# Kernel tuning notes

Hardware: AMD Instinct MI355X
Metric: run time of the kernel (lower is better)

Reference implementation:

```python
import jax, jax.numpy as jnp
import numpy as np

N, E, G = 20000, 100000, 32
HID, HEADS, HC = 64, 8, 64  # hidden, heads, per-head channels (PyG: out_channels per head)
L, K = 3, 4


def setup_inputs() -> dict:
    key = jax.random.key(0)
    ks = jax.random.split(key, 20)
    rn = lambda k, s, sc=0.05: jax.random.normal(k, s, jnp.float32) * sc
    HO = HEADS * HC  # 512
    return {
        "x": jax.random.uniform(ks[0], (N, 7), jnp.float32),
        "edge_attr": jax.random.normal(ks[1], (E, 4), jnp.float32),
        "means": jax.random.normal(ks[2], (K, 8), jnp.float32),
        "log_stds": jnp.zeros((K, 8), jnp.float32),
        "sp_W": rn(ks[3], (K, HID), 0.3), "sp_b": jnp.zeros((HID,), jnp.float32),
        "ne_W": rn(ks[4], (7, HID), 0.3), "ne_b": jnp.zeros((HID,), jnp.float32),
        "ee_W": rn(ks[5], (4, HID), 0.3), "ee_b": jnp.zeros((HID,), jnp.float32),
        "Wq": rn(ks[6], (L, HID, HO)), "bq": jnp.zeros((L, HO), jnp.float32),
        "Wk": rn(ks[7], (L, HID, HO)), "bk": jnp.zeros((L, HO), jnp.float32),
        "Wv": rn(ks[8], (L, HID, HO)), "bv": jnp.zeros((L, HO), jnp.float32),
        "We": rn(ks[9], (L, HID, HO)), "be": jnp.zeros((L, HO), jnp.float32),
        "Ws": rn(ks[10], (L, HID, HID)), "bs": jnp.zeros((L, HID), jnp.float32),
        "eu_W": rn(ks[11], (L, 3 * HID, HID)), "eu_b": jnp.zeros((L, HID), jnp.float32),
        "rW1": rn(ks[12], (2 * HID, HID)), "rb1": jnp.zeros((HID,), jnp.float32),
        "rW2": rn(ks[13], (HID, HID)), "rb2": jnp.zeros((HID,), jnp.float32),
        "rW3": rn(ks[14], (HID, 2)), "rb3": jnp.zeros((2,), jnp.float32),
        "edge_index": jax.random.randint(ks[15], (2, E), 0, N, jnp.int32),
        "batch": jnp.sort(jax.random.randint(ks[16], (N,), 0, G, jnp.int32)),
        "num_graphs": G,
    }


def reference(x, edge_attr, means, log_stds, sp_W, sp_b, ne_W, ne_b, ee_W, ee_b,
              Wq, bq, Wk, bk, Wv, bv, We, be, Ws, bs, eu_W, eu_b,
              rW1, rb1, rW2, rb2, rW3, rb3, edge_index, batch, num_graphs):
    n = x.shape[0]
    src, dst = edge_index[0], edge_index[1]

    # ---- SpatialGaussianEncoder (dropout is identity in eval) ----
    p = x[:, :4]
    sl, sr = p[src, :2], p[src, 2:4]
    dl, dr = p[dst, :2], p[dst, 2:4]
    rel = jnp.stack([dl - sl, dl - sr, dr - sl, dr - sr], axis=1)  # [E,4,2]
    dist = jnp.linalg.norm(rel, axis=-1)                           # [E,4]
    ang = jnp.arctan2(rel[..., 1], rel[..., 0])                    # [E,4]
    u = jnp.stack([dist, ang], axis=-1).reshape(-1, 8)             # [E,8] (d,a)x4
    std = jnp.exp(log_stds) + 1e-6                                 # [K,8]
    z = (u[:, None, :] - means[None]) / std[None]                  # [E,K,8]
    w = jnp.exp(-0.5 * jnp.sum(z * z, axis=-1))                    # [E,K]
    sp = jax.nn.relu(w @ sp_W + sp_b)                              # [E,HID]

    h = jax.nn.relu(x @ ne_W + ne_b)                               # [N,HID]
    ea = jax.nn.relu(edge_attr @ ee_W + ee_b) + sp                 # [E,HID]

    scale = 1.0 / float(np.sqrt(HC))
    for l in range(L):
        # PyG TransformerConv(hidden, hidden, heads=8, edge_dim=hidden, concat=False)
        q = (h @ Wq[l] + bq[l]).reshape(n, HEADS, HC)
        k = (h @ Wk[l] + bk[l]).reshape(n, HEADS, HC)
        v = (h @ Wv[l] + bv[l]).reshape(n, HEADS, HC)
        e = (ea @ We[l] + be[l]).reshape(-1, HEADS, HC)
        kj = k[src] + e                                            # [E,H,C]
        alpha = jnp.einsum('ehc,ehc->eh', q[dst], kj) * scale      # [E,H]
        m = jax.ops.segment_max(alpha, dst, num_segments=n)
        ex = jnp.exp(alpha - m[dst])
        den = jax.ops.segment_sum(ex, dst, num_segments=n)
        a = ex / (den[dst] + 1e-16)                                # scatter-softmax over dst
        msg = a[:, :, None] * (v[src] + e)                         # [E,H,C]
        out = jax.ops.segment_sum(msg, dst, num_segments=n).mean(axis=1)  # concat=False -> head mean
        h = jax.nn.relu(out + h @ Ws[l] + bs[l])                   # skip (root_weight) + F.relu
        ef = jnp.concatenate([h[src], h[dst], ea], axis=1)         # [E,3*HID]
        ea = jax.nn.relu(ef @ eu_W[l] + eu_b[l])

    # ---- per-graph masked-mean pooling == segment mean ----
    cn = jnp.maximum(jax.ops.segment_sum(jnp.ones((n,), x.dtype), batch, num_segments=num_graphs), 1.0)
    node_pool = jax.ops.segment_sum(h, batch, num_segments=num_graphs) / cn[:, None]
    eb = batch[src]
    ce = jnp.maximum(jax.ops.segment_sum(jnp.ones((src.shape[0],), x.dtype), eb, num_segments=num_graphs), 1.0)
    edge_pool = jax.ops.segment_sum(ea, eb, num_segments=num_graphs) / ce[:, None]
    g = jnp.concatenate([node_pool, edge_pool], axis=1)            # [G,2*HID]

    h1 = jax.nn.relu(g @ rW1 + rb1)
    h2 = jax.nn.relu(h1 @ rW2 + rb2)
    return jnp.tanh(h2 @ rW3 + rb3)                                # [G,2]
```

## Files before the change

### kernel.cpp

```cpp
#include <hip/hip_runtime.h>
#include <hip/hip_bf16.h>
#include <cstdint>
#include <cstddef>



__global__ void __launch_bounds__(256) k_node_embed(
    const float* __restrict__ x, const float* __restrict__ neW, const float* __restrict__ neb,
    float* __restrict__ h, int N)
{
    int idx = blockIdx.x * 256 + threadIdx.x;
    int n = idx >> 6, c = idx & 63;
    if (n >= N) return;
    float acc = neb[c];
    #pragma unroll
    for (int j = 0; j < 7; ++j) acc += x[(size_t)n * 7 + j] * neW[j * 64 + c];
    h[(size_t)n * 64 + c] = fmaxf(acc, 0.f);
}

__global__ void __launch_bounds__(256) k_edge_w(
    const float* __restrict__ x,
    const float* __restrict__ means, const float* __restrict__ log_stds,
    const int* __restrict__ src, const int* __restrict__ dst,
    float* __restrict__ wbuf, int E)
{
    int e = blockIdx.x * 256 + threadIdx.x;
    if (e >= E) return;
    int s = src[e], d = dst[e];
    const float* ps = x + (size_t)s * 7;
    const float* pd = x + (size_t)d * 7;
    float slx = ps[0], sly = ps[1], srx = ps[2], sry = ps[3];
    float dlx = pd[0], dly = pd[1], drx = pd[2], dry = pd[3];
    float u[8];
    float rx, ry;
    rx = dlx - slx; ry = dly - sly; u[0] = sqrtf(rx*rx + ry*ry); u[1] = atan2f(ry, rx);
    rx = dlx - srx; ry = dly - sry; u[2] = sqrtf(rx*rx + ry*ry); u[3] = atan2f(ry, rx);
    rx = drx - slx; ry = dry - sly; u[4] = sqrtf(rx*rx + ry*ry); u[5] = atan2f(ry, rx);
    rx = drx - srx; ry = dry - sry; u[6] = sqrtf(rx*rx + ry*ry); u[7] = atan2f(ry, rx);
    #pragma unroll
    for (int kk = 0; kk < 4; ++kk) {
        float ssum = 0.f;
        #pragma unroll
        for (int dd = 0; dd < 8; ++dd) {
            float stdv = expf(log_stds[kk*8+dd]) + 1e-6f;
            float z = (u[dd] - means[kk*8+dd]) / stdv;
            ssum += z * z;
        }
        wbuf[(size_t)e*4 + kk] = expf(-0.5f * ssum);
    }
}

__global__ void __launch_bounds__(256) k_edge_ea(
    const float* __restrict__ edge_attr, const float* __restrict__ wbuf,
    const float* __restrict__ spW, const float* __restrict__ spb,
    const float* __restrict__ eeW, const float* __restrict__ eeb,
    float* __restrict__ ea, int E)
{
    int idx = blockIdx.x * 256 + threadIdx.x;
    int e = idx >> 6, c = idx & 63;
    if (e >= E) return;
    float acce = eeb[c];
    #pragma unroll
    for (int j = 0; j < 4; ++j) acce += edge_attr[(size_t)e*4 + j] * eeW[j*64 + c];
    float accs = spb[c];
    #pragma unroll
    for (int j = 0; j < 4; ++j) accs += wbuf[(size_t)e*4 + j] * spW[j*64 + c];
    ea[(size_t)e*64 + c] = fmaxf(acce, 0.f) + fmaxf(accs, 0.f);
}


__global__ void __launch_bounds__(256) k_hist(
    const int* __restrict__ dst, int* __restrict__ deg, int E)
{
    int e = blockIdx.x * 256 + threadIdx.x;
    if (e < E) atomicAdd(deg + dst[e], 1);
}

__global__ void __launch_bounds__(1024) k_scan(
    const int* __restrict__ deg, int* __restrict__ ptr, int* __restrict__ headw, int N)
{
    __shared__ int part[1024];
    int t = threadIdx.x;
    int per = (N + 1023) / 1024;
    int s = 0;
    for (int i = 0; i < per; ++i) { int idx = t*per + i; if (idx < N) s += deg[idx]; }
    part[t] = s;
    __syncthreads();
    for (int off = 1; off < 1024; off <<= 1) {
        int v = (t >= off) ? part[t - off] : 0;
        __syncthreads();
        part[t] += v;
        __syncthreads();
    }
    int base = (t > 0) ? part[t - 1] : 0;
    for (int i = 0; i < per; ++i) {
        int idx = t*per + i;
        if (idx < N) { ptr[idx] = base; headw[idx] = base; base += deg[idx]; }
    }
    if (t == 1023) ptr[N] = part[1023];
}

__global__ void __launch_bounds__(256) k_scatter(
    const int* __restrict__ dst, const int* __restrict__ src, const int* __restrict__ batch,
    int* __restrict__ headw, int* __restrict__ perm, int* __restrict__ srcg,
    int* __restrict__ ieb, int E)
{
    int e = blockIdx.x * 256 + threadIdx.x;
    if (e < E) {
        int s = src[e];
        int pos = atomicAdd(headw + dst[e], 1);
        perm[pos] = e;
        srcg[pos] = s;
        ieb[e] = batch[s];
    }
}


__global__ void __launch_bounds__(256) k_wprod_all(
    const float* __restrict__ Wq, const float* __restrict__ bq,
    const float* __restrict__ Wk, const float* __restrict__ We,
    float* __restrict__ Mk, float* __restrict__ Me,
    float* __restrict__ bqk, float* __restrict__ bqe)
{
    int h = blockIdx.x;
    int which = blockIdx.y;
    int l = blockIdx.z;
    const float* Wq_l = Wq + (size_t)l * 64 * 512;
    const float* bq_l = bq + (size_t)l * 512;
    const float* Wx_l = (which ? We : Wk) + (size_t)l * 64 * 512;
    float* M  = (which ? Me : Mk) + (size_t)l * 64 * 512;
    float* bM = (which ? bqe : bqk) + (size_t)l * 512;
    __shared__ float wq_s[65][64];
    __shared__ float wx_s[64][65];
    int tid = threadIdx.x;
    for (int i = tid; i < 4096; i += 256) {
        int r = i >> 6, c2 = i & 63;
        wq_s[r][c2] = Wq_l[(size_t)r*512 + h*64 + c2];
        wx_s[r][c2] = Wx_l[(size_t)r*512 + h*64 + c2];
    }
    if (tid < 64) wq_s[64][tid] = bq_l[h*64 + tid];
    __syncthreads();
    int j = tid & 63, cg = tid >> 6;
    for (int c = cg*16; c < cg*16 + 16; ++c) {
        float s = 0.f;
        #pragma unroll 8
        for (int c2 = 0; c2 < 64; ++c2) s += wq_s[c][c2] * wx_s[j][c2];
        M[(size_t)c*512 + h*64 + j] = s;
    }
    if (tid < 64) {
        float s = 0.f;
        #pragma unroll 8
        for (int c2 = 0; c2 < 64; ++c2) s += wq_s[64][c2] * wx_s[tid][c2];
        bM[h*64 + tid] = s;
    }
}

__global__ void __launch_bounds__(64) k_wqb_all(
    const float* __restrict__ Wq, const float* __restrict__ bq,
    const float* __restrict__ bk, const float* __restrict__ be,
    float* __restrict__ wqb, float* __restrict__ cb)
{
    int l = blockIdx.x;
    const float* Wq_l = Wq + (size_t)l * 64 * 512;
    const float* bq_l = bq + (size_t)l * 512;
    const float* bk_l = bk + (size_t)l * 512;
    const float* be_l = be + (size_t)l * 512;
    float* wqb_l = wqb + (size_t)l * 512;
    float* cb_l  = cb + (size_t)l * 8;
    int c = threadIdx.x;
    for (int h = 0; h < 8; ++h) {
        float s = 0.f;
        for (int c2 = 0; c2 < 64; ++c2)
            s += Wq_l[(size_t)c*512 + h*64 + c2] * (bk_l[h*64+c2] + be_l[h*64+c2]);
        wqb_l[c*8 + h] = s;
    }
    if (c < 8) {
        float s = 0.f;
        for (int c2 = 0; c2 < 64; ++c2)
            s += bq_l[c*64 + c2] * (bk_l[c*64+c2] + be_l[c*64+c2]);
        cb_l[c] = s;
    }
}

__global__ void __launch_bounds__(256) k_qb(
    const float* __restrict__ h, const float* __restrict__ wqb, const float* __restrict__ cb,
    float* __restrict__ qbv, int N)
{
    int idx = blockIdx.x * 256 + threadIdx.x;
    int n = idx >> 3, hh = idx & 7;
    if (n >= N) return;
    float s = cb[hh];
    #pragma unroll 8
    for (int c = 0; c < 64; ++c) s += h[(size_t)n*64 + c] * wqb[c*8 + hh];
    qbv[(size_t)n*8 + hh] = s;
}


__global__ void __launch_bounds__(256) k_gemm512_r32(
    const float* __restrict__ X, const float* __restrict__ W, const float* __restrict__ bias,
    float* __restrict__ Y, int M)
{
    __shared__ __align__(16) float xs[32][64];
    int tid = threadIdx.x;
    int r0 = blockIdx.x * 32;
    for (int i = tid; i < 2048; i += 256) {
        int r = i >> 6, c = i & 63;
        int rr = r0 + r;
        xs[r][c] = (rr < M) ? X[(size_t)rr * 64 + c] : 0.f;
    }
    __syncthreads();
    int wv = tid >> 6, lane = tid & 63;
    int c0 = lane * 8;
    float acc[8][8];
    float4 b0 = *(const float4*)(bias + c0);
    float4 b1 = *(const float4*)(bias + c0 + 4);
    #pragma unroll
    for (int t = 0; t < 8; ++t) {
        acc[t][0]=b0.x; acc[t][1]=b0.y; acc[t][2]=b0.z; acc[t][3]=b0.w;
        acc[t][4]=b1.x; acc[t][5]=b1.y; acc[t][6]=b1.z; acc[t][7]=b1.w;
    }
    #pragma unroll 2
    for (int j = 0; j < 64; ++j) {
        float4 wa = *(const float4*)(W + (size_t)j*512 + c0);
        float4 wb = *(const float4*)(W + (size_t)j*512 + c0 + 4);
        #pragma unroll
        for (int t = 0; t < 8; ++t) {
            float a = xs[wv*8 + t][j];
            acc[t][0] += a*wa.x; acc[t][1] += a*wa.y; acc[t][2] += a*wa.z; acc[t][3] += a*wa.w;
            acc[t][4] += a*wb.x; acc[t][5] += a*wb.y; acc[t][6] += a*wb.z; acc[t][7] += a*wb.w;
        }
    }
    #pragma unroll
    for (int t = 0; t < 8; ++t) {
        int r = r0 + wv*8 + t;
        if (r < M) {
            float4 o0 = {acc[t][0],acc[t][1],acc[t][2],acc[t][3]};
            float4 o1 = {acc[t][4],acc[t][5],acc[t][6],acc[t][7]};
            *(float4*)(Y + (size_t)r*512 + c0)     = o0;
            *(float4*)(Y + (size_t)r*512 + c0 + 4) = o1;
        }
    }
}


__global__ void __launch_bounds__(256) k_attn_alpha2(
    const float* __restrict__ qk, const float* __restrict__ qe2, const float* __restrict__ qbv,
    const float* __restrict__ ea, const float* __restrict__ hbuf,
    const int* __restrict__ ptr, const int* __restrict__ perm, const int* __restrict__ srcg,
    float* __restrict__ alpha, float* __restrict__ mbuf, float* __restrict__ dbuf, int N)
{
    int wv = threadIdx.x >> 6, lane = threadIdx.x & 63;
    int n = blockIdx.x * 4 + wv;
    if (n >= N) return;
    int h = lane >> 3, p = lane & 7;
    int b = ptr[n], e_ = ptr[n + 1];
    const float4* xp = (const float4*)(qk + (size_t)n*512 + lane*8);
    float4 x0 = xp[0], x1 = xp[1];
    const float4* gp = (const float4*)(qe2 + (size_t)n*512 + lane*8);
    float4 g0 = gp[0], g1 = gp[1];
    float qbh = qbv[(size_t)n*8 + h];
    float m = -3.4e38f, den = 0.f;
    for (int it = b; it < e_; ++it) {
        int s = srcg[it];
        int e = perm[it];
        const float4* hp = (const float4*)(hbuf + (size_t)s*64 + p*8);
        float4 h0 = hp[0], h1 = hp[1];
        const float4* ap = (const float4*)(ea + (size_t)e*64 + p*8);
        float4 a0 = ap[0], a1 = ap[1];
        float t = x0.x*h0.x + x0.y*h0.y + x0.z*h0.z + x0.w*h0.w
                + x1.x*h1.x + x1.y*h1.y + x1.z*h1.z + x1.w*h1.w
                + g0.x*a0.x + g0.y*a0.y + g0.z*a0.z + g0.w*a0.w
                + g1.x*a1.x + g1.y*a1.y + g1.z*a1.z + g1.w*a1.w;
        t += __shfl_xor(t, 1);
        t += __shfl_xor(t, 2);
        t += __shfl_xor(t, 4);
        float al = 0.125f * (t + qbh);
        float mn = fmaxf(m, al);
        den = den * expf(m - mn) + expf(al - mn);
        m = mn;
        if (p == 0) alpha[(size_t)it*8 + h] = al;
    }
    if (p == 0) {
        mbuf[(size_t)n*8 + h] = m;
        dbuf[(size_t)n*8 + h] = den;
    }
}

__global__ void __launch_bounds__(256) k_attn_agg2(
    const float* __restrict__ alpha, const float* __restrict__ mbuf, const float* __restrict__ dbuf,
    const float* __restrict__ ea, const float* __restrict__ hbuf,
    const int* __restrict__ ptr, const int* __restrict__ perm, const int* __restrict__ srcg,
    float* __restrict__ hagg, float* __restrict__ tbuf, float* __restrict__ sbuf, int N)
{
    int wv = threadIdx.x >> 6, lane = threadIdx.x & 63;
    int n = blockIdx.x * 4 + wv;
    if (n >= N) return;
    int h = lane >> 3, p = lane & 7;
    int b = ptr[n], e_ = ptr[n + 1];
    float m = mbuf[(size_t)n*8 + h];
    float inv = 0.125f / (dbuf[(size_t)n*8 + h] + 1e-16f);
    float hacc[8], tacc[8];
    #pragma unroll
    for (int i = 0; i < 8; ++i) { hacc[i] = 0.f; tacc[i] = 0.f; }
    float sacc = 0.f;
    for (int it = b; it < e_; ++it) {
        int s = srcg[it];
        int e = perm[it];
        float a = expf(alpha[(size_t)it*8 + h] - m) * inv;
        sacc += a;
        const float4* hp = (const float4*)(hbuf + (size_t)s*64 + p*8);
        float4 h0 = hp[0], h1 = hp[1];
        const float4* ap = (const float4*)(ea + (size_t)e*64 + p*8);
        float4 a0 = ap[0], a1 = ap[1];
        hacc[0] += a*h0.x; hacc[1] += a*h0.y; hacc[2] += a*h0.z; hacc[3] += a*h0.w;
        hacc[4] += a*h1.x; hacc[5] += a*h1.y; hacc[6] += a*h1.z; hacc[7] += a*h1.w;
        tacc[0] += a*a0.x; tacc[1] += a*a0.y; tacc[2] += a*a0.z; tacc[3] += a*a0.w;
        tacc[4] += a*a1.x; tacc[5] += a*a1.y; tacc[6] += a*a1.z; tacc[7] += a*a1.w;
    }
    float4 o;
    o = {hacc[0],hacc[1],hacc[2],hacc[3]}; *(float4*)(hagg + (size_t)n*512 + lane*8)     = o;
    o = {hacc[4],hacc[5],hacc[6],hacc[7]}; *(float4*)(hagg + (size_t)n*512 + lane*8 + 4) = o;
    o = {tacc[0],tacc[1],tacc[2],tacc[3]}; *(float4*)(tbuf + (size_t)n*512 + lane*8)     = o;
    o = {tacc[4],tacc[5],tacc[6],tacc[7]}; *(float4*)(tbuf + (size_t)n*512 + lane*8 + 4) = o;
    if (p == 0) sbuf[(size_t)n*8 + h] = sacc;
}

__global__ void __launch_bounds__(256) k_nf_gemm2(
    const float* __restrict__ tbuf, const float* __restrict__ hagg,
    const float* __restrict__ We, const float* __restrict__ Wv,
    float* __restrict__ pbuf, int N)
{
    __shared__ float As[64][132];
    __shared__ __align__(16) float Wt[64][64];
    int tid = threadIdx.x;
    int y = blockIdx.y;
    int n0 = blockIdx.x * 128;
    int wv = tid >> 6, lane = tid & 63;
    int rg = lane >> 3, cg = lane & 7;
    int c0 = cg * 8;
    int rbase = wv * 32 + rg * 4;
    float acc[4][8];
    #pragma unroll
    for (int t = 0; t < 4; ++t)
        #pragma unroll
        for (int i = 0; i < 8; ++i) acc[t][i] = 0.f;
    #pragma unroll
    for (int round = 0; round < 2; ++round) {
        const float* A = round ? hagg : tbuf;
        const float* W = round ? Wv : We;
        {
            int rt = tid & 127;
            int n = n0 + rt;
            int jh = (tid >> 7) * 32;
            if (n < N) {
                const float* ap = A + (size_t)n*512 + y*64;
                #pragma unroll
                for (int j4 = 0; j4 < 8; ++j4) {
                    int j = jh + j4 * 4;
                    float4 a = *(const float4*)(ap + j);
                    As[j+0][rt] = a.x; As[j+1][rt] = a.y;
                    As[j+2][rt] = a.z; As[j+3][rt] = a.w;
                }
            } else {
                #pragma unroll
                for (int j4 = 0; j4 < 8; ++j4) {
                    int j = jh + j4 * 4;
                    As[j+0][rt] = 0.f; As[j+1][rt] = 0.f;
                    As[j+2][rt] = 0.f; As[j+3][rt] = 0.f;
                }
            }
            #pragma unroll
            for (int i = 0; i < 4; ++i) {
                int idx = tid + i * 256;
                int j = idx >> 4, c4 = (idx & 15) * 4;
                *(float4*)&Wt[j][c4] = *(const float4*)(W + (size_t)j*512 + y*64 + c4);
            }
        }
        __syncthreads();
        #pragma unroll 4
        for (int j = 0; j < 64; ++j) {
            float4 av = *(const float4*)&As[j][rbase];
            float4 w0 = *(const float4*)&Wt[j][c0];
            float4 w1 = *(const float4*)&Wt[j][c0 + 4];
            acc[0][0] += av.x*w0.x; acc[0][1] += av.x*w0.y; acc[0][2] += av.x*w0.z; acc[0][3] += av.x*w0.w;
            acc[0][4] += av.x*w1.x; acc[0][5] += av.x*w1.y; acc[0][6] += av.x*w1.z; acc[0][7] += av.x*w1.w;
            acc[1][0] += av.y*w0.x; acc[1][1] += av.y*w0.y; acc[1][2] += av.y*w0.z; acc[1][3] += av.y*w0.w;
            acc[1][4] += av.y*w1.x; acc[1][5] += av.y*w1.y; acc[1][6] += av.y*w1.z; acc[1][7] += av.y*w1.w;
            acc[2][0] += av.z*w0.x; acc[2][1] += av.z*w0.y; acc[2][2] += av.z*w0.z; acc[2][3] += av.z*w0.w;
            acc[2][4] += av.z*w1.x; acc[2][5] += av.z*w1.y; acc[2][6] += av.z*w1.z; acc[2][7] += av.z*w1.w;
            acc[3][0] += av.w*w0.x; acc[3][1] += av.w*w0.y; acc[3][2] += av.w*w0.z; acc[3][3] += av.w*w0.w;
            acc[3][4] += av.w*w1.x; acc[3][5] += av.w*w1.y; acc[3][6] += av.w*w1.z; acc[3][7] += av.w*w1.w;
        }
        __syncthreads();
    }
    float* out = pbuf + (size_t)y * N * 64;
    #pragma unroll
    for (int t = 0; t < 4; ++t) {
        int n = n0 + rbase + t;
        if (n < N) {
            float4 o0 = {acc[t][0],acc[t][1],acc[t][2],acc[t][3]};
            float4 o1 = {acc[t][4],acc[t][5],acc[t][6],acc[t][7]};
            *(float4*)(out + (size_t)n*64 + c0)     = o0;
            *(float4*)(out + (size_t)n*64 + c0 + 4) = o1;
        }
    }
}

__global__ void __launch_bounds__(256) k_nf_reduce2(
    const float* __restrict__ pbuf, const float* __restrict__ hin,
    const float* __restrict__ sbuf, const float* __restrict__ Ws,
    const float* __restrict__ be, const float* __restrict__ bv,
    const float* __restrict__ bs, float* __restrict__ hnext, int N)
{
    int idx = blockIdx.x * 256 + threadIdx.x;
    int n = idx >> 6, cc = idx & 63;
    if (n >= N) return;
    float a = bs[cc];
    #pragma unroll
    for (int y = 0; y < 8; ++y) a += pbuf[(size_t)y*N*64 + (size_t)n*64 + cc];
    float hv = hin[(size_t)n*64 + cc];
    #pragma unroll 8
    for (int j = 0; j < 64; ++j) a += __shfl(hv, j) * Ws[(size_t)j*64 + cc];
    #pragma unroll
    for (int h = 0; h < 8; ++h)
        a += sbuf[(size_t)n*8 + h] * (be[h*64 + cc] + bv[h*64 + cc]);
    hnext[(size_t)n*64 + cc] = fmaxf(a, 0.f);
}

__global__ void __launch_bounds__(256) k_eu_pre(
    const float* __restrict__ h, const float* __restrict__ euW,
    float* __restrict__ hw, int N)
{
    __shared__ float As[64][132];
    __shared__ __align__(16) float Wt[64][64];
    int tid = threadIdx.x;
    int y = blockIdx.y;
    int n0 = blockIdx.x * 128;
    {
        int rt = tid & 127;
        int n = n0 + rt;
        int jh = (tid >> 7) * 32;
        if (n < N) {
            const float* ap = h + (size_t)n*64;
            #pragma unroll
            for (int j4 = 0; j4 < 8; ++j4) {
                int j = jh + j4 * 4;
                float4 a = *(const float4*)(ap + j);
                As[j+0][rt] = a.x; As[j+1][rt] = a.y;
                As[j+2][rt] = a.z; As[j+3][rt] = a.w;
            }
        } else {
            #pragma unroll
            for (int j4 = 0; j4 < 8; ++j4) {
                int j = jh + j4 * 4;
                As[j+0][rt] = 0.f; As[j+1][rt] = 0.f;
                As[j+2][rt] = 0.f; As[j+3][rt] = 0.f;
            }
        }
        #pragma unroll
        for (int i = 0; i < 4; ++i) {
            int idx = tid + i * 256;
            *(float4*)&Wt[idx >> 4][(idx & 15) * 4] =
                *(const float4*)(euW + (size_t)y*4096 + idx * 4);
        }
    }
    __syncthreads();
    int wv = tid >> 6, lane = tid & 63;
    int rg = lane >> 3, cg = lane & 7;
    int c0 = cg * 8;
    int rbase = wv * 32 + rg * 4;
    float acc[4][8];
    #pragma unroll
    for (int t = 0; t < 4; ++t)
        #pragma unroll
        for (int i = 0; i < 8; ++i) acc[t][i] = 0.f;
    #pragma unroll 4
    for (int j = 0; j < 64; ++j) {
        float4 av = *(const float4*)&As[j][rbase];
        float4 w0 = *(const float4*)&Wt[j][c0];
        float4 w1 = *(const float4*)&Wt[j][c0 + 4];
        acc[0][0] += av.x*w0.x; acc[0][1] += av.x*w0.y; acc[0][2] += av.x*w0.z; acc[0][3] += av.x*w0.w;
        acc[0][4] += av.x*w1.x; acc[0][5] += av.x*w1.y; acc[0][6] += av.x*w1.z; acc[0][7] += av.x*w1.w;
        acc[1][0] += av.y*w0.x; acc[1][1] += av.y*w0.y; acc[1][2] += av.y*w0.z; acc[1][3] += av.y*w0.w;
        acc[1][4] += av.y*w1.x; acc[1][5] += av.y*w1.y; acc[1][6] += av.y*w1.z; acc[1][7] += av.y*w1.w;
        acc[2][0] += av.z*w0.x; acc[2][1] += av.z*w0.y; acc[2][2] += av.z*w0.z; acc[2][3] += av.z*w0.w;
        acc[2][4] += av.z*w1.x; acc[2][5] += av.z*w1.y; acc[2][6] += av.z*w1.z; acc[2][7] += av.z*w1.w;
        acc[3][0] += av.w*w0.x; acc[3][1] += av.w*w0.y; acc[3][2] += av.w*w0.z; acc[3][3] += av.w*w0.w;
        acc[3][4] += av.w*w1.x; acc[3][5] += av.w*w1.y; acc[3][6] += av.w*w1.z; acc[3][7] += av.w*w1.w;
    }
    #pragma unroll
    for (int t = 0; t < 4; ++t) {
        int n = n0 + rbase + t;
        if (n < N) {
            float4 o0 = {acc[t][0],acc[t][1],acc[t][2],acc[t][3]};
            float4 o1 = {acc[t][4],acc[t][5],acc[t][6],acc[t][7]};
            *(float4*)(hw + (size_t)n*128 + y*64 + c0)     = o0;
            *(float4*)(hw + (size_t)n*128 + y*64 + c0 + 4) = o1;
        }
    }
}

__global__ void __launch_bounds__(256) k_edge_update2(
    const float* __restrict__ hw, const float* __restrict__ ea,
    const float* __restrict__ euW2, const float* __restrict__ eub,
    const int* __restrict__ src, const int* __restrict__ dst,
    float* __restrict__ ea2, int E)
{
    __shared__ float As[64][132];
    __shared__ __align__(16) float Wt[64][64];
    __shared__ int sid[128], did[128];
    int tid = threadIdx.x;
    int e0 = blockIdx.x * 128;
    if (tid < 128) {
        int e = e0 + tid; if (e >= E) e = E - 1;
        sid[tid] = src[e]; did[tid] = dst[e];
    }
    {
        int et = tid & 127;
        int e = e0 + et; if (e >= E) e = E - 1;
        const float* ap = ea + (size_t)e * 64;
        int jh = (tid >> 7) * 32;
        #pragma unroll
        for (int j4 = 0; j4 < 8; ++j4) {
            int j = jh + j4 * 4;
            float4 a = *(const float4*)(ap + j);
            As[j+0][et] = a.x; As[j+1][et] = a.y;
            As[j+2][et] = a.z; As[j+3][et] = a.w;
        }
        #pragma unroll
        for (int i = 0; i < 4; ++i) {
            int idx = tid + i * 256;
            *(float4*)&Wt[idx >> 4][(idx & 15) * 4] = *(const float4*)(euW2 + idx * 4);
        }
    }
    __syncthreads();
    int wv = tid >> 6, lane = tid & 63;
    int rg = lane >> 3, cg = lane & 7;
    int c0 = cg * 8;
    int rbase = wv * 32 + rg * 4;
    float acc[4][8];
    float4 b0 = *(const float4*)(eub + c0);
    float4 b1 = *(const float4*)(eub + c0 + 4);
    #pragma unroll
    for (int t = 0; t < 4; ++t) {
        acc[t][0]=b0.x; acc[t][1]=b0.y; acc[t][2]=b0.z; acc[t][3]=b0.w;
        acc[t][4]=b1.x; acc[t][5]=b1.y; acc[t][6]=b1.z; acc[t][7]=b1.w;
    }
    #pragma unroll 4
    for (int j = 0; j < 64; ++j) {
        float4 av = *(const float4*)&As[j][rbase];
        float4 w0 = *(const float4*)&Wt[j][c0];
        float4 w1 = *(const float4*)&Wt[j][c0 + 4];
        acc[0][0] += av.x*w0.x; acc[0][1] += av.x*w0.y; acc[0][2] += av.x*w0.z; acc[0][3] += av.x*w0.w;
        acc[0][4] += av.x*w1.x; acc[0][5] += av.x*w1.y; acc[0][6] += av.x*w1.z; acc[0][7] += av.x*w1.w;
        acc[1][0] += av.y*w0.x; acc[1][1] += av.y*w0.y; acc[1][2] += av.y*w0.z; acc[1][3] += av.y*w0.w;
        acc[1][4] += av.y*w1.x; acc[1][5] += av.y*w1.y; acc[1][6] += av.y*w1.z; acc[1][7] += av.y*w1.w;
        acc[2][0] += av.z*w0.x; acc[2][1] += av.z*w0.y; acc[2][2] += av.z*w0.z; acc[2][3] += av.z*w0.w;
        acc[2][4] += av.z*w1.x; acc[2][5] += av.z*w1.y; acc[2][6] += av.z*w1.z; acc[2][7] += av.z*w1.w;
        acc[3][0] += av.w*w0.x; acc[3][1] += av.w*w0.y; acc[3][2] += av.w*w0.z; acc[3][3] += av.w*w0.w;
        acc[3][4] += av.w*w1.x; acc[3][5] += av.w*w1.y; acc[3][6] += av.w*w1.z; acc[3][7] += av.w*w1.w;
    }
    #pragma unroll
    for (int t = 0; t < 4; ++t) {
        int e = e0 + rbase + t;
        if (e < E) {
            int s = sid[rbase + t], d = did[rbase + t];
            const float4* sp = (const float4*)(hw + (size_t)s*128 + c0);
            const float4* dp = (const float4*)(hw + (size_t)d*128 + 64 + c0);
            float4 s0 = sp[0], s1 = sp[1];
            float4 d0 = dp[0], d1 = dp[1];
            float4 o0 = {fmaxf(acc[t][0]+s0.x+d0.x,0.f), fmaxf(acc[t][1]+s0.y+d0.y,0.f),
                         fmaxf(acc[t][2]+s0.z+d0.z,0.f), fmaxf(acc[t][3]+s0.w+d0.w,0.f)};
            float4 o1 = {fmaxf(acc[t][4]+s1.x+d1.x,0.f), fmaxf(acc[t][5]+s1.y+d1.y,0.f),
                         fmaxf(acc[t][6]+s1.z+d1.z,0.f), fmaxf(acc[t][7]+s1.w+d1.w,0.f)};
            *(float4*)(ea2 + (size_t)e*64 + c0)     = o0;
            *(float4*)(ea2 + (size_t)e*64 + c0 + 4) = o1;
        }
    }
}


__global__ void __launch_bounds__(64) k_node_pool(
    const float* __restrict__ h, const int* __restrict__ batch,
    float* __restrict__ npool, float* __restrict__ cn, int N)
{
    int lane = threadIdx.x;
    int n0 = blockIdx.x * 64;
    float acc = 0.f; int cur = -1; int run = 0;
    for (int i = 0; i < 64; ++i) {
        int n = n0 + i;
        if (n >= N) break;
        int b = batch[n];
        if (b != cur) {
            if (cur >= 0) {
                atomicAdd(npool + (size_t)cur*64 + lane, acc);
                if (lane == 0) atomicAdd(cn + cur, (float)run);
            }
            cur = b; acc = 0.f; run = 0;
        }
        acc += h[(size_t)n*64 + lane];
        ++run;
    }
    if (cur >= 0) {
        atomicAdd(npool + (size_t)cur*64 + lane, acc);
        if (lane == 0) atomicAdd(cn + cur, (float)run);
    }
}

__global__ void __launch_bounds__(256) k_edge_pool2(
    const float* __restrict__ ea, const int* __restrict__ ieb,
    float* __restrict__ rep, int E)
{
    __shared__ float pool_s[32][64];
    __shared__ float cnt_s[32];
    int tid = threadIdx.x;
    for (int i = tid; i < 2048; i += 256) ((float*)pool_s)[i] = 0.f;
    if (tid < 32) cnt_s[tid] = 0.f;
    __syncthreads();
    int wv = tid >> 6, lane = tid & 63;
    int base = blockIdx.x * 64 + wv * 16;
    int b16[16]; float v16[16];
    #pragma unroll
    for (int u = 0; u < 16; ++u) {
        int e = base + u;
        bool ok = (e < E);
        b16[u] = ok ? ieb[e] : -1;
        v16[u] = ok ? ea[(size_t)e*64 + lane] : 0.f;
    }
    #pragma unroll
    for (int u = 0; u < 16; ++u) {
        if (b16[u] >= 0) {
            atomicAdd(&pool_s[b16[u]][lane], v16[u]);
            if (lane == 0) atomicAdd(&cnt_s[b16[u]], 1.f);
        }
    }
    __syncthreads();
    float* myrep = rep + (size_t)(blockIdx.x & 7) * 2080;
    for (int i = tid; i < 2048; i += 256) atomicAdd(myrep + i, ((float*)pool_s)[i]);
    if (tid < 32) atomicAdd(myrep + 2048 + tid, cnt_s[tid]);
}

__global__ void __launch_bounds__(256) k_pool_merge(
    const float* __restrict__ rep, float* __restrict__ epool, float* __restrict__ ce)
{
    int i = blockIdx.x * 256 + threadIdx.x;
    if (i < 2080) {
        float s = 0.f;
        #pragma unroll
        for (int r = 0; r < 8; ++r) s += rep[(size_t)r*2080 + i];
        if (i < 2048) epool[i] = s; else ce[i - 2048] = s;
    }
}

__global__ void __launch_bounds__(64) k_head_mlp(
    const float* __restrict__ npool, const float* __restrict__ epool,
    const float* __restrict__ cn, const float* __restrict__ ce,
    const float* __restrict__ rW1, const float* __restrict__ rb1,
    const float* __restrict__ rW2, const float* __restrict__ rb2,
    const float* __restrict__ rW3, const float* __restrict__ rb3,
    float* __restrict__ out)
{
    __shared__ float g[128];
    __shared__ float h1[64];
    __shared__ float h2[64];
    int b = blockIdx.x, lane = threadIdx.x;
    float cnv = fmaxf(cn[b], 1.f), cev = fmaxf(ce[b], 1.f);
    g[lane]      = npool[(size_t)b*64 + lane] / cnv;
    g[64 + lane] = epool[(size_t)b*64 + lane] / cev;
    __syncthreads();
    float acc = rb1[lane];
    #pragma unroll 4
    for (int j = 0; j < 128; ++j) acc += g[j] * rW1[j*64 + lane];
    h1[lane] = fmaxf(acc, 0.f);
    __syncthreads();
    acc = rb2[lane];
    #pragma unroll 4
    for (int j = 0; j < 64; ++j) acc += h1[j] * rW2[j*64 + lane];
    h2[lane] = fmaxf(acc, 0.f);
    __syncthreads();
    if (lane < 2) {
        float o = rb3[lane];
        for (int j = 0; j < 64; ++j) o += h2[j] * rW3[j*2 + lane];
        out[b*2 + lane] = tanhf(o);
    }
}


extern "C" void kernel_launch(void* const* d_in, const int* in_sizes, int n_in,
                              void* d_out, int out_size, void* d_ws, size_t ws_size,
                              hipStream_t stream)
{
    const float* x         = (const float*)d_in[0];
    const float* edge_attr = (const float*)d_in[1];
    const float* means     = (const float*)d_in[2];
    const float* log_stds  = (const float*)d_in[3];
    const float* spW       = (const float*)d_in[4];
    const float* spb       = (const float*)d_in[5];
    const float* neW       = (const float*)d_in[6];
    const float* neb       = (const float*)d_in[7];
    const float* eeW       = (const float*)d_in[8];
    const float* eeb       = (const float*)d_in[9];
    const float* Wq        = (const float*)d_in[10];
    const float* bq        = (const float*)d_in[11];
    const float* Wk        = (const float*)d_in[12];
    const float* bk        = (const float*)d_in[13];
    const float* Wv        = (const float*)d_in[14];
    const float* bv        = (const float*)d_in[15];
    const float* We        = (const float*)d_in[16];
    const float* be        = (const float*)d_in[17];
    const float* Ws        = (const float*)d_in[18];
    const float* bs        = (const float*)d_in[19];
    const float* euW       = (const float*)d_in[20];
    const float* eub       = (const float*)d_in[21];
    const float* rW1       = (const float*)d_in[22];
    const float* rb1       = (const float*)d_in[23];
    const float* rW2       = (const float*)d_in[24];
    const float* rb2       = (const float*)d_in[25];
    const float* rW3       = (const float*)d_in[26];
    const float* rb3       = (const float*)d_in[27];
    const int* eidx        = (const int*)d_in[28];
    const int* batch       = (const int*)d_in[29];

    int N = in_sizes[0] / 7;
    int E = in_sizes[1] / 4;
    const int G = 32;
    const int* srcp = eidx;
    const int* dstp = eidx + E;

    float* ws = (float*)d_ws;
    size_t fl = 0;
    float* hA    = ws + fl; fl += (size_t)N * 64;
    float* hB    = ws + fl; fl += (size_t)N * 64;
    float* eaA   = ws + fl; fl += (size_t)E * 64;
    float* eaB   = ws + fl; fl += (size_t)E * 64;
    float* B1    = ws + fl; fl += (size_t)N * 512;
    float* B2    = ws + fl; fl += (size_t)N * 512;
    float* B3    = ws + fl; fl += (size_t)N * 512;
    float* alpha = ws + fl; fl += (size_t)E * 8;
    float* mbuf  = ws + fl; fl += (size_t)N * 8;
    float* dbuf  = ws + fl; fl += (size_t)N * 8;
    float* sbuf  = ws + fl; fl += (size_t)N * 8;
    float* qbv   = ws + fl; fl += (size_t)N * 8;
    float* npool = ws + fl; fl += (size_t)G * 64;
    float* epool = ws + fl; fl += (size_t)G * 64;
    float* cn    = ws + fl; fl += G;
    float* ce    = ws + fl; fl += G;
    float* Mk3   = ws + fl; fl += 3 * 64 * 512;
    float* Me3   = ws + fl; fl += 3 * 64 * 512;
    float* bqk3  = ws + fl; fl += 3 * 512;
    float* bqe3  = ws + fl; fl += 3 * 512;
    float* wqb3  = ws + fl; fl += 3 * 512;
    float* cb3   = ws + fl; fl += 24;
    float* rep   = ws + fl; fl += 8 * 2080;
    int* ideg  = (int*)(ws + fl); fl += (size_t)N;
    int* iptr  = (int*)(ws + fl); fl += (size_t)N + 1;
    int* ihead = (int*)(ws + fl); fl += (size_t)N;
    int* iperm = (int*)(ws + fl); fl += (size_t)E;
    int* isrcg = (int*)(ws + fl); fl += (size_t)E;
    int* ieb   = (int*)(ws + fl); fl += (size_t)E;

    float* wbuf = alpha;

    hipMemsetAsync(npool, 0, (size_t)(G * 130) * sizeof(float), stream);
    hipMemsetAsync(rep, 0, (size_t)(8 * 2080) * sizeof(float), stream);
    hipMemsetAsync(ideg, 0, (size_t)N * sizeof(int), stream);

    k_node_embed<<<(N * 64 + 255) / 256, 256, 0, stream>>>(x, neW, neb, hA, N);
    k_edge_w<<<(E + 255) / 256, 256, 0, stream>>>(x, means, log_stds, srcp, dstp, wbuf, E);
    k_edge_ea<<<((size_t)E * 64 + 255) / 256, 256, 0, stream>>>(edge_attr, wbuf,
                                                                spW, spb, eeW, eeb, eaA, E);
    k_hist<<<(E + 255) / 256, 256, 0, stream>>>(dstp, ideg, E);
    k_scan<<<1, 1024, 0, stream>>>(ideg, iptr, ihead, N);
    k_scatter<<<(E + 255) / 256, 256, 0, stream>>>(dstp, srcp, batch, ihead, iperm, isrcg, ieb, E);
    k_wprod_all<<<dim3(8, 2, 3), 256, 0, stream>>>(Wq, bq, Wk, We, Mk3, Me3, bqk3, bqe3);
    k_wqb_all<<<3, 64, 0, stream>>>(Wq, bq, bk, be, wqb3, cb3);

    float* hcur = hA;  float* hnext = hB;
    float* eacur = eaA; float* eanext = eaB;
    for (int l = 0; l < 3; ++l) {
        const float* Wv_l = Wv + (size_t)l * 64 * 512;
        const float* We_l = We + (size_t)l * 64 * 512;
        const float* bv_l = bv + (size_t)l * 512;
        const float* be_l = be + (size_t)l * 512;
        const float* euW_l = euW + (size_t)l * 192 * 64;

        k_gemm512_r32<<<(N + 31) / 32, 256, 0, stream>>>(hcur, Mk3 + (size_t)l * 32768,
                                                         bqk3 + (size_t)l * 512, B1, N);
        k_gemm512_r32<<<(N + 31) / 32, 256, 0, stream>>>(hcur, Me3 + (size_t)l * 32768,
                                                         bqe3 + (size_t)l * 512, B2, N);
        k_qb<<<((size_t)N * 8 + 255) / 256, 256, 0, stream>>>(hcur, wqb3 + (size_t)l * 512,
                                                              cb3 + (size_t)l * 8, qbv, N);

        k_attn_alpha2<<<(N + 3) / 4, 256, 0, stream>>>(B1, B2, qbv, eacur, hcur,
                                                       iptr, iperm, isrcg,
                                                       alpha, mbuf, dbuf, N);
        k_attn_agg2<<<(N + 3) / 4, 256, 0, stream>>>(alpha, mbuf, dbuf, eacur, hcur,
                                                     iptr, iperm, isrcg,
                                                     B1 , B2 , sbuf, N);
        k_nf_gemm2<<<dim3((N + 127) / 128, 8), 256, 0, stream>>>(B2, B1, We_l, Wv_l, B3, N);
        k_nf_reduce2<<<((size_t)N * 64 + 255) / 256, 256, 0, stream>>>(B3, hcur, sbuf,
                                                                       Ws + (size_t)l * 64 * 64,
                                                                       be_l, bv_l,
                                                                       bs + (size_t)l * 64,
                                                                       hnext, N);
        k_eu_pre<<<dim3((N + 127) / 128, 2), 256, 0, stream>>>(hnext, euW_l, B3, N);
        k_edge_update2<<<(E + 127) / 128, 256, 0, stream>>>(B3, eacur, euW_l + 2 * 4096,
                                                            eub + (size_t)l * 64,
                                                            srcp, dstp, eanext, E);
        float* t1 = hcur; hcur = hnext; hnext = t1;
        float* t2 = eacur; eacur = eanext; eanext = t2;
    }

    k_node_pool<<<(N + 63) / 64, 64, 0, stream>>>(hcur, batch, npool, cn, N);
    k_edge_pool2<<<(E + 63) / 64, 256, 0, stream>>>(eacur, ieb, rep, E);
    k_pool_merge<<<9, 256, 0, stream>>>(rep, epool, ce);
    k_head_mlp<<<G, 64, 0, stream>>>(npool, epool, cn, ce, rW1, rb1, rW2, rb2, rW3, rb3,
                                     (float*)d_out);
}
```

Baseline: 875.8 us.

## Fuse attention alpha and aggregation with online softmax, merge GEMM launches

Merges the two-pass attention (alpha/max/denominator, then weighted aggregation) into one kernel. It uses online-softmax rescaling of the accumulators, so the gathers of source h and edge features happen once per edge instead of twice, and the alpha/m/den round trips disappear. The two 512-wide projection GEMMs become one launch using blockIdx.y. The node-feature GEMM now covers two head slices per block, so the reduce step reads four partial buffers instead of eight. In exchange the inner loop does extra rescale multiplies on 16 accumulators per edge and has fewer blocks for the GEMM.

```diff
diff --git a/kernel.cpp b/kernel.cpp
--- a/kernel.cpp
+++ b/kernel.cpp
@@ -196,10 +196,15 @@
 }
 
 
-__global__ void __launch_bounds__(256) k_gemm512_r32(
-    const float* __restrict__ X, const float* __restrict__ W, const float* __restrict__ bias,
-    float* __restrict__ Y, int M)
-{
+__global__ void __launch_bounds__(256) k_gemm512_dual(
+    const float* __restrict__ X,
+    const float* __restrict__ W0, const float* __restrict__ b0p, float* __restrict__ Y0,
+    const float* __restrict__ W1, const float* __restrict__ b1p, float* __restrict__ Y1,
+    int M)
+{
+    const float* W    = blockIdx.y ? W1 : W0;
+    const float* bias = blockIdx.y ? b1p : b0p;
+    float* Y          = blockIdx.y ? Y1 : Y0;
     __shared__ __align__(16) float xs[32][64];
     int tid = threadIdx.x;
     int r0 = blockIdx.x * 32;
@@ -243,11 +248,11 @@
 }
 
 
-__global__ void __launch_bounds__(256) k_attn_alpha2(
+__global__ void __launch_bounds__(256) k_attn_fused(
     const float* __restrict__ qk, const float* __restrict__ qe2, const float* __restrict__ qbv,
     const float* __restrict__ ea, const float* __restrict__ hbuf,
     const int* __restrict__ ptr, const int* __restrict__ perm, const int* __restrict__ srcg,
-    float* __restrict__ alpha, float* __restrict__ mbuf, float* __restrict__ dbuf, int N)
+    float* __restrict__ hagg, float* __restrict__ tbuf, float* __restrict__ sbuf, int N)
 {
     int wv = threadIdx.x >> 6, lane = threadIdx.x & 63;
     int n = blockIdx.x * 4 + wv;
@@ -260,6 +265,9 @@
     float4 g0 = gp[0], g1 = gp[1];
     float qbh = qbv[(size_t)n*8 + h];
     float m = -3.4e38f, den = 0.f;
+    float hacc[8], tacc[8];
+    #pragma unroll
+    for (int i = 0; i < 8; ++i) { hacc[i] = 0.f; tacc[i] = 0.f; }
     for (int it = b; it < e_; ++it) {
         int s = srcg[it];
         int e = perm[it];
@@ -276,53 +284,30 @@
         t += __shfl_xor(t, 4);
         float al = 0.125f * (t + qbh);
         float mn = fmaxf(m, al);
-        den = den * expf(m - mn) + expf(al - mn);
+        float r = expf(m - mn);
+        float w = expf(al - mn);
+        den = den * r + w;
         m = mn;
-        if (p == 0) alpha[(size_t)it*8 + h] = al;
-    }
-    if (p == 0) {
-        mbuf[(size_t)n*8 + h] = m;
-        dbuf[(size_t)n*8 + h] = den;
-    }
-}
-
-__global__ void __launch_bounds__(256) k_attn_agg2(
-    const float* __restrict__ alpha, const float* __restrict__ mbuf, const float* __restrict__ dbuf,
-    const float* __restrict__ ea, const float* __restrict__ hbuf,
-    const int* __restrict__ ptr, const int* __restrict__ perm, const int* __restrict__ srcg,
-    float* __restrict__ hagg, float* __restrict__ tbuf, float* __restrict__ sbuf, int N)
-{
-    int wv = threadIdx.x >> 6, lane = threadIdx.x & 63;
-    int n = blockIdx.x * 4 + wv;
-    if (n >= N) return;
-    int h = lane >> 3, p = lane & 7;
-    int b = ptr[n], e_ = ptr[n + 1];
-    float m = mbuf[(size_t)n*8 + h];
-    float inv = 0.125f / (dbuf[(size_t)n*8 + h] + 1e-16f);
-    float hacc[8], tacc[8];
-    #pragma unroll
-    for (int i = 0; i < 8; ++i) { hacc[i] = 0.f; tacc[i] = 0.f; }
-    float sacc = 0.f;
-    for (int it = b; it < e_; ++it) {
-        int s = srcg[it];
-        int e = perm[it];
-        float a = expf(alpha[(size_t)it*8 + h] - m) * inv;
-        sacc += a;
-        const float4* hp = (const float4*)(hbuf + (size_t)s*64 + p*8);
-        float4 h0 = hp[0], h1 = hp[1];
-        const float4* ap = (const float4*)(ea + (size_t)e*64 + p*8);
-        float4 a0 = ap[0], a1 = ap[1];
-        hacc[0] += a*h0.x; hacc[1] += a*h0.y; hacc[2] += a*h0.z; hacc[3] += a*h0.w;
-        hacc[4] += a*h1.x; hacc[5] += a*h1.y; hacc[6] += a*h1.z; hacc[7] += a*h1.w;
-        tacc[0] += a*a0.x; tacc[1] += a*a0.y; tacc[2] += a*a0.z; tacc[3] += a*a0.w;
-        tacc[4] += a*a1.x; tacc[5] += a*a1.y; tacc[6] += a*a1.z; tacc[7] += a*a1.w;
-    }
+        hacc[0] = hacc[0]*r + w*h0.x; hacc[1] = hacc[1]*r + w*h0.y;
+        hacc[2] = hacc[2]*r + w*h0.z; hacc[3] = hacc[3]*r + w*h0.w;
+        hacc[4] = hacc[4]*r + w*h1.x; hacc[5] = hacc[5]*r + w*h1.y;
+        hacc[6] = hacc[6]*r + w*h1.z; hacc[7] = hacc[7]*r + w*h1.w;
+        tacc[0] = tacc[0]*r + w*a0.x; tacc[1] = tacc[1]*r + w*a0.y;
+        tacc[2] = tacc[2]*r + w*a0.z; tacc[3] = tacc[3]*r + w*a0.w;
+        tacc[4] = tacc[4]*r + w*a1.x; tacc[5] = tacc[5]*r + w*a1.y;
+        tacc[6] = tacc[6]*r + w*a1.z; tacc[7] = tacc[7]*r + w*a1.w;
+    }
+    float inv = 0.125f / (den + 1e-16f);
     float4 o;
-    o = {hacc[0],hacc[1],hacc[2],hacc[3]}; *(float4*)(hagg + (size_t)n*512 + lane*8)     = o;
-    o = {hacc[4],hacc[5],hacc[6],hacc[7]}; *(float4*)(hagg + (size_t)n*512 + lane*8 + 4) = o;
-    o = {tacc[0],tacc[1],tacc[2],tacc[3]}; *(float4*)(tbuf + (size_t)n*512 + lane*8)     = o;
-    o = {tacc[4],tacc[5],tacc[6],tacc[7]}; *(float4*)(tbuf + (size_t)n*512 + lane*8 + 4) = o;
-    if (p == 0) sbuf[(size_t)n*8 + h] = sacc;
+    o = {hacc[0]*inv,hacc[1]*inv,hacc[2]*inv,hacc[3]*inv};
+    *(float4*)(hagg + (size_t)n*512 + lane*8)     = o;
+    o = {hacc[4]*inv,hacc[5]*inv,hacc[6]*inv,hacc[7]*inv};
+    *(float4*)(hagg + (size_t)n*512 + lane*8 + 4) = o;
+    o = {tacc[0]*inv,tacc[1]*inv,tacc[2]*inv,tacc[3]*inv};
+    *(float4*)(tbuf + (size_t)n*512 + lane*8)     = o;
+    o = {tacc[4]*inv,tacc[5]*inv,tacc[6]*inv,tacc[7]*inv};
+    *(float4*)(tbuf + (size_t)n*512 + lane*8 + 4) = o;
+    if (p == 0) sbuf[(size_t)n*8 + h] = den * inv;
 }
 
 __global__ void __launch_bounds__(256) k_nf_gemm2(
@@ -333,7 +318,7 @@
     __shared__ float As[64][132];
     __shared__ __align__(16) float Wt[64][64];
     int tid = threadIdx.x;
-    int y = blockIdx.y;
+    int g = blockIdx.y;
     int n0 = blockIdx.x * 128;
     int wv = tid >> 6, lane = tid & 63;
     int rg = lane >> 3, cg = lane & 7;
@@ -345,55 +330,59 @@
         #pragma unroll
         for (int i = 0; i < 8; ++i) acc[t][i] = 0.f;
     #pragma unroll
-    for (int round = 0; round < 2; ++round) {
-        const float* A = round ? hagg : tbuf;
-        const float* W = round ? Wv : We;
-        {
-            int rt = tid & 127;
-            int n = n0 + rt;
-            int jh = (tid >> 7) * 32;
-            if (n < N) {
-                const float* ap = A + (size_t)n*512 + y*64;
+    for (int yy = 0; yy < 2; ++yy) {
+        int y = g * 2 + yy;
+        #pragma unroll
+        for (int round = 0; round < 2; ++round) {
+            const float* A = round ? hagg : tbuf;
+            const float* W = round ? Wv : We;
+            {
+                int rt = tid & 127;
+                int n = n0 + rt;
+                int jh = (tid >> 7) * 32;
+                if (n < N) {
+                    const float* ap = A + (size_t)n*512 + y*64;
+                    #pragma unroll
+                    for (int j4 = 0; j4 < 8; ++j4) {
+                        int j = jh + j4 * 4;
+                        float4 a = *(const float4*)(ap + j);
+                        As[j+0][rt] = a.x; As[j+1][rt] = a.y;
+                        As[j+2][rt] = a.z; As[j+3][rt] = a.w;
+                    }
+                } else {
+                    #pragma unroll
+                    for (int j4 = 0; j4 < 8; ++j4) {
+                        int j = jh + j4 * 4;
+                        As[j+0][rt] = 0.f; As[j+1][rt] = 0.f;
+                        As[j+2][rt] = 0.f; As[j+3][rt] = 0.f;
+                    }
+                }
                 #pragma unroll
-                for (int j4 = 0; j4 < 8; ++j4) {
-                    int j = jh + j4 * 4;
-                    float4 a = *(const float4*)(ap + j);
-                    As[j+0][rt] = a.x; As[j+1][rt] = a.y;
-                    As[j+2][rt] = a.z; As[j+3][rt] = a.w;
-                }
-            } else {
-                #pragma unroll
-                for (int j4 = 0; j4 < 8; ++j4) {
-                    int j = jh + j4 * 4;
-                    As[j+0][rt] = 0.f; As[j+1][rt] = 0.f;
-                    As[j+2][rt] = 0.f; As[j+3][rt] = 0.f;
+                for (int i = 0; i < 4; ++i) {
+                    int idx = tid + i * 256;
+                    int j = idx >> 4, c4 = (idx & 15) * 4;
+                    *(float4*)&Wt[j][c4] = *(const float4*)(W + (size_t)j*512 + y*64 + c4);
                 }
             }
-            #pragma unroll
-            for (int i = 0; i < 4; ++i) {
-                int idx = tid + i * 256;
-                int j = idx >> 4, c4 = (idx & 15) * 4;
-                *(float4*)&Wt[j][c4] = *(const float4*)(W + (size_t)j*512 + y*64 + c4);
+            __syncthreads();
+            #pragma unroll 4
+            for (int j = 0; j < 64; ++j) {
+                float4 av = *(const float4*)&As[j][rbase];
+                float4 w0 = *(const float4*)&Wt[j][c0];
+                float4 w1 = *(const float4*)&Wt[j][c0 + 4];
+                acc[0][0] += av.x*w0.x; acc[0][1] += av.x*w0.y; acc[0][2] += av.x*w0.z; acc[0][3] += av.x*w0.w;
+                acc[0][4] += av.x*w1.x; acc[0][5] += av.x*w1.y; acc[0][6] += av.x*w1.z; acc[0][7] += av.x*w1.w;
+                acc[1][0] += av.y*w0.x; acc[1][1] += av.y*w0.y; acc[1][2] += av.y*w0.z; acc[1][3] += av.y*w0.w;
+                acc[1][4] += av.y*w1.x; acc[1][5] += av.y*w1.y; acc[1][6] += av.y*w1.z; acc[1][7] += av.y*w1.w;
+                acc[2][0] += av.z*w0.x; acc[2][1] += av.z*w0.y; acc[2][2] += av.z*w0.z; acc[2][3] += av.z*w0.w;
+                acc[2][4] += av.z*w1.x; acc[2][5] += av.z*w1.y; acc[2][6] += av.z*w1.z; acc[2][7] += av.z*w1.w;
+                acc[3][0] += av.w*w0.x; acc[3][1] += av.w*w0.y; acc[3][2] += av.w*w0.z; acc[3][3] += av.w*w0.w;
+                acc[3][4] += av.w*w1.x; acc[3][5] += av.w*w1.y; acc[3][6] += av.w*w1.z; acc[3][7] += av.w*w1.w;
             }
-        }
-        __syncthreads();
-        #pragma unroll 4
-        for (int j = 0; j < 64; ++j) {
-            float4 av = *(const float4*)&As[j][rbase];
-            float4 w0 = *(const float4*)&Wt[j][c0];
-            float4 w1 = *(const float4*)&Wt[j][c0 + 4];
-            acc[0][0] += av.x*w0.x; acc[0][1] += av.x*w0.y; acc[0][2] += av.x*w0.z; acc[0][3] += av.x*w0.w;
-            acc[0][4] += av.x*w1.x; acc[0][5] += av.x*w1.y; acc[0][6] += av.x*w1.z; acc[0][7] += av.x*w1.w;
-            acc[1][0] += av.y*w0.x; acc[1][1] += av.y*w0.y; acc[1][2] += av.y*w0.z; acc[1][3] += av.y*w0.w;
-            acc[1][4] += av.y*w1.x; acc[1][5] += av.y*w1.y; acc[1][6] += av.y*w1.z; acc[1][7] += av.y*w1.w;
-            acc[2][0] += av.z*w0.x; acc[2][1] += av.z*w0.y; acc[2][2] += av.z*w0.z; acc[2][3] += av.z*w0.w;
-            acc[2][4] += av.z*w1.x; acc[2][5] += av.z*w1.y; acc[2][6] += av.z*w1.z; acc[2][7] += av.z*w1.w;
-            acc[3][0] += av.w*w0.x; acc[3][1] += av.w*w0.y; acc[3][2] += av.w*w0.z; acc[3][3] += av.w*w0.w;
-            acc[3][4] += av.w*w1.x; acc[3][5] += av.w*w1.y; acc[3][6] += av.w*w1.z; acc[3][7] += av.w*w1.w;
-        }
-        __syncthreads();
-    }
-    float* out = pbuf + (size_t)y * N * 64;
+            __syncthreads();
+        }
+    }
+    float* out = pbuf + (size_t)g * N * 64;
     #pragma unroll
     for (int t = 0; t < 4; ++t) {
         int n = n0 + rbase + t;
@@ -417,7 +406,7 @@
     if (n >= N) return;
     float a = bs[cc];
     #pragma unroll
-    for (int y = 0; y < 8; ++y) a += pbuf[(size_t)y*N*64 + (size_t)n*64 + cc];
+    for (int y = 0; y < 4; ++y) a += pbuf[(size_t)y*N*64 + (size_t)n*64 + cc];
     float hv = hin[(size_t)n*64 + cc];
     #pragma unroll 8
     for (int j = 0; j < 64; ++j) a += __shfl(hv, j) * Ws[(size_t)j*64 + cc];
@@ -737,8 +726,6 @@
     float* B2    = ws + fl; fl += (size_t)N * 512;
     float* B3    = ws + fl; fl += (size_t)N * 512;
     float* alpha = ws + fl; fl += (size_t)E * 8;
-    float* mbuf  = ws + fl; fl += (size_t)N * 8;
-    float* dbuf  = ws + fl; fl += (size_t)N * 8;
     float* sbuf  = ws + fl; fl += (size_t)N * 8;
     float* qbv   = ws + fl; fl += (size_t)N * 8;
     float* npool = ws + fl; fl += (size_t)G * 64;
@@ -784,20 +771,17 @@
         const float* be_l = be + (size_t)l * 512;
         const float* euW_l = euW + (size_t)l * 192 * 64;
 
-        k_gemm512_r32<<<(N + 31) / 32, 256, 0, stream>>>(hcur, Mk3 + (size_t)l * 32768,
-                                                         bqk3 + (size_t)l * 512, B1, N);
-        k_gemm512_r32<<<(N + 31) / 32, 256, 0, stream>>>(hcur, Me3 + (size_t)l * 32768,
-                                                         bqe3 + (size_t)l * 512, B2, N);
+        k_gemm512_dual<<<dim3((N + 31) / 32, 2), 256, 0, stream>>>(
+            hcur,
+            Mk3 + (size_t)l * 32768, bqk3 + (size_t)l * 512, B1,
+            Me3 + (size_t)l * 32768, bqe3 + (size_t)l * 512, B2, N);
         k_qb<<<((size_t)N * 8 + 255) / 256, 256, 0, stream>>>(hcur, wqb3 + (size_t)l * 512,
                                                               cb3 + (size_t)l * 8, qbv, N);
 
-        k_attn_alpha2<<<(N + 3) / 4, 256, 0, stream>>>(B1, B2, qbv, eacur, hcur,
-                                                       iptr, iperm, isrcg,
-                                                       alpha, mbuf, dbuf, N);
-        k_attn_agg2<<<(N + 3) / 4, 256, 0, stream>>>(alpha, mbuf, dbuf, eacur, hcur,
-                                                     iptr, iperm, isrcg,
-                                                     B1 , B2 , sbuf, N);
-        k_nf_gemm2<<<dim3((N + 127) / 128, 8), 256, 0, stream>>>(B2, B1, We_l, Wv_l, B3, N);
+        k_attn_fused<<<(N + 3) / 4, 256, 0, stream>>>(B1, B2, qbv, eacur, hcur,
+                                                      iptr, iperm, isrcg,
+                                                      B1 , B2 , sbuf, N);
+        k_nf_gemm2<<<dim3((N + 127) / 128, 4), 256, 0, stream>>>(B2, B1, We_l, Wv_l, B3, N);
         k_nf_reduce2<<<((size_t)N * 64 + 255) / 256, 256, 0, stream>>>(B3, hcur, sbuf,
                                                                        Ws + (size_t)l * 64 * 64,
                                                                        be_l, bv_l,
```

New measurement: 763.0 us. 1.15x faster.
